# Kernel tuning notes

Hardware: AMD Instinct MI355X
Metric: run time of the kernel (lower is better)

## Reference

```python
import jax, jax.numpy as jnp
import numpy as np

N = 100000      # nodes
E = 1600000     # edges (no self loops; GATv2Conv adds them)
D_NODE = 256    # node_embedding_depth
D_MSG = 128     # message_depth
D_RBF = 32      # radial_dim
H = 8           # heads
D_HEAD = D_MSG // H


def setup_inputs() -> dict:
    key = jax.random.key(0)
    ks = jax.random.split(key, 12)
    x = jax.random.normal(ks[0], (N, D_NODE), dtype=jnp.float32)
    rbf = jax.random.uniform(ks[1], (E, D_RBF), dtype=jnp.float32)
    # edges with no self loops: src = (dst + r) % N, r in [1, N)
    dst = jax.random.randint(ks[2], (E,), 0, N)
    r = jax.random.randint(ks[3], (E,), 1, N)
    src = (dst + r) % N
    edge_index = jnp.stack([src, dst]).astype(jnp.int64)
    batch = jnp.zeros((N,), dtype=jnp.int64)
    s = 0.05
    W_n2m = jax.random.normal(ks[4], (D_MSG, D_NODE), dtype=jnp.float32) * s
    W_r2m = jax.random.normal(ks[5], (D_MSG, D_RBF), dtype=jnp.float32) * s
    Wl = jax.random.normal(ks[6], (D_MSG, D_MSG), dtype=jnp.float32) * s
    bl = jnp.zeros((D_MSG,), dtype=jnp.float32)
    Wr = jax.random.normal(ks[7], (D_MSG, D_MSG), dtype=jnp.float32) * s
    br = jnp.zeros((D_MSG,), dtype=jnp.float32)
    We = jax.random.normal(ks[8], (D_MSG, D_MSG), dtype=jnp.float32) * s
    att = jax.random.normal(ks[9], (H, D_HEAD), dtype=jnp.float32) * s
    bias = jnp.zeros((D_MSG,), dtype=jnp.float32)
    W_m2n = jax.random.normal(ks[10], (D_NODE, D_MSG), dtype=jnp.float32) * s
    return {"x": x, "rbf": rbf, "edge_index": edge_index, "batch": batch,
            "W_n2m": W_n2m, "W_r2m": W_r2m, "Wl": Wl, "bl": bl, "Wr": Wr,
            "br": br, "We": We, "att": att, "bias": bias, "W_m2n": W_m2n}


def reference(x, rbf, edge_index, batch, W_n2m, W_r2m, Wl, bl, Wr, br, We, att, bias, W_m2n):
    n = x.shape[0]
    h, d = att.shape
    # node_to_message / radial_to_message (norm=None -> identity Normalization)
    xm = x @ W_n2m.T                      # [N, D_MSG]
    ea = rbf @ W_r2m.T                    # [E, D_MSG]
    src, dst = edge_index[0], edge_index[1]
    # GATv2Conv add_self_loops with fill_value='mean': self-loop edge_attr is
    # the mean of incoming edge attrs per target node (0 if none).
    deg = jax.ops.segment_sum(jnp.ones((ea.shape[0],), ea.dtype), dst, num_segments=n)
    loop_attr = jax.ops.segment_sum(ea, dst, num_segments=n) / jnp.maximum(deg, 1.0)[:, None]
    loop_idx = jnp.arange(n, dtype=src.dtype)
    src_f = jnp.concatenate([src, loop_idx])
    dst_f = jnp.concatenate([dst, loop_idx])
    ea_f = jnp.concatenate([ea, loop_attr], axis=0)   # [E+N, D_MSG]
    # GATv2 attention
    xl = (xm @ Wl.T + bl).reshape(n, h, d)            # source transform
    xr = (xm @ Wr.T + br).reshape(n, h, d)            # target transform
    e = (ea_f @ We.T).reshape(-1, h, d)               # edge transform
    u = jax.nn.leaky_relu(xl[src_f] + xr[dst_f] + e, 0.2)  # [E+N, H, d]
    logits = jnp.einsum('ehd,hd->eh', u, att)         # [E+N, H]
    # segment softmax over incoming edges per target node (self loops guarantee non-empty)
    mx = jax.ops.segment_max(logits, dst_f, num_segments=n)
    p = jnp.exp(logits - mx[dst_f])
    denom = jax.ops.segment_sum(p, dst_f, num_segments=n)
    alpha = p / denom[dst_f]                          # [E+N, H]
    msg = xl[src_f] * alpha[:, :, None]               # [E+N, H, d]
    out = jax.ops.segment_sum(msg, dst_f, num_segments=n).reshape(n, h * d) + bias
    return out @ W_m2n.T                              # [N, D_NODE]
```

## Files before the change

### kernel.cpp

```cpp
#include <hip/hip_runtime.h>
#include <cstdint>
#include <cstddef>

#define N_NODES 100000
#define N_EDGES 1600000

#define M_PAD 100096
#define SCAN_NB 98
#define CH 16

#define OFF_XLR    ((size_t)0)
#define OFF_XB     (OFF_XLR    + (size_t)N_NODES*256)
#define OFF_ACCB   (OFF_XB     + (size_t)12812288)
#define OFF_CSRS   (OFF_ACCB   + (size_t)6406144)
#define OFF_CSRE   (OFF_CSRS   + (size_t)N_EDGES)
#define OFF_ROW    (OFF_CSRE   + (size_t)N_EDGES)
#define OFF_CNT    (OFF_ROW    + (size_t)100016)
#define OFF_DEGI   (OFF_CNT    + (size_t)N_NODES)
#define OFF_BSUMS  (OFF_DEGI   + (size_t)N_NODES)
#define OFF_BCAT   (OFF_BSUMS  + 128)
#define OFF_WCOMBB (OFF_BCAT   + 256)
#define OFF_WCATB  (OFF_WCOMBB + 2048)
#define OFF_WM2NB  (OFF_WCATB  + 32768)

typedef __attribute__((ext_vector_type(8))) short short8;
typedef __attribute__((ext_vector_type(4))) float float4v;

__device__ __forceinline__ unsigned short f2bf(float f) {
  unsigned u = __float_as_uint(f);
  unsigned r = (u + 0x7fff + ((u >> 16) & 1)) >> 16;
  return (unsigned short)r;
}

__global__ void k_zero(float* __restrict__ p, size_t n4) {
  size_t i = (size_t)blockIdx.x * blockDim.x + threadIdx.x;
  size_t stride = (size_t)gridDim.x * blockDim.x;
  float4 z = make_float4(0.f, 0.f, 0.f, 0.f);
  for (; i < n4; i += stride) ((float4*)p)[i] = z;
}

__global__ void k_convx(const float* __restrict__ x, unsigned short* __restrict__ xb, unsigned n4) {
  unsigned i = blockIdx.x * blockDim.x + threadIdx.x;
  unsigned stride = gridDim.x * blockDim.x;
  for (; i < n4; i += stride) {
    float4 v = ((const float4*)x)[i];
    ushort4 o;
    o.x = f2bf(v.x); o.y = f2bf(v.y); o.z = f2bf(v.z); o.w = f2bf(v.w);
    ((ushort4*)xb)[i] = o;
  }
}

__global__ void k_weights(const float* __restrict__ Wl, const float* __restrict__ Wr,
                          const float* __restrict__ We, const float* __restrict__ W_n2m,
                          const float* __restrict__ W_r2m, const float* __restrict__ bl,
                          const float* __restrict__ br, const float* __restrict__ W_m2n,
                          unsigned short* __restrict__ WcatB, float* __restrict__ bcat,
                          unsigned short* __restrict__ WcombB, unsigned short* __restrict__ Wm2nB) {
  int idx = blockIdx.x * blockDim.x + threadIdx.x;
  if (idx < 65536) {
    int o = idx >> 8, i = idx & 255;
    const float* wrow = (o < 128) ? (Wl + o * 128) : (Wr + (o - 128) * 128);
    float s = 0.f;
    for (int k = 0; k < 128; ++k) s += wrow[k] * W_n2m[k * 256 + i];
    WcatB[idx] = f2bf(s);
  } else if (idx < 65536 + 256) {
    int o = idx - 65536;
    bcat[o] = (o < 128) ? bl[o] : br[o - 128];
  } else if (idx < 65536 + 256 + 4096) {
    int q = idx - (65536 + 256);
    int j = q >> 7, o = q & 127;
    float s = 0.f;
    for (int k = 0; k < 128; ++k) s += We[o * 128 + k] * W_r2m[k * 32 + j];
    WcombB[o * 32 + j] = f2bf(s);
  } else if (idx < 65536 + 256 + 4096 + 32768) {
    int q = idx - (65536 + 256 + 4096);
    Wm2nB[q] = f2bf(W_m2n[q]);
  }
}

template <bool HAS_BIAS>
__global__ __launch_bounds__(256) void gemm_mfma(const unsigned short* __restrict__ A,
                                                 const unsigned short* __restrict__ B,
                                                 const float* __restrict__ bias,
                                                 float* __restrict__ C,
                                                 int M, int NC, int K) {
  __shared__ short As[128 * 32];
  __shared__ short Bs[128 * 32];
  const int tid = threadIdx.x;
  const int lane = tid & 63;
  const int wv = tid >> 6;
  const int rowBase = blockIdx.x << 7;
  const int colBase = blockIdx.y << 7;
  const int wrow = (wv & 1) << 6;
  const int wcol = (wv >> 1) << 6;

  const int srow = tid >> 2;
  const int skc = (tid & 3) << 3;

  const int n0 = lane & 15;
  const int q = lane >> 4;

  float4v acc[4][4];
#pragma unroll
  for (int i = 0; i < 4; ++i)
#pragma unroll
    for (int j = 0; j < 4; ++j) acc[i][j] = (float4v)(0.f);

  for (int k0 = 0; k0 < K; k0 += 32) {
    const unsigned aoff0 = (unsigned)(rowBase + srow) * K + k0 + skc;
    const unsigned aoff1 = (unsigned)(rowBase + 64 + srow) * K + k0 + skc;
    const unsigned boff0 = (unsigned)(colBase + srow) * K + k0 + skc;
    const unsigned boff1 = (unsigned)(colBase + 64 + srow) * K + k0 + skc;
    uint4 a0 = *(const uint4*)(A + aoff0);
    uint4 a1 = *(const uint4*)(A + aoff1);
    uint4 b0 = *(const uint4*)(B + boff0);
    uint4 b1 = *(const uint4*)(B + boff1);
    __syncthreads();
    ((uint4*)As)[tid] = a0;
    ((uint4*)As)[256 + tid] = a1;
    ((uint4*)Bs)[tid] = b0;
    ((uint4*)Bs)[256 + tid] = b1;
    __syncthreads();

    short8 af[4], bf[4];
    const short8* Ap = (const short8*)As;
    const short8* Bp = (const short8*)Bs;
#pragma unroll
    for (int i = 0; i < 4; ++i) af[i] = Ap[(wrow + i * 16 + n0) * 4 + q];
#pragma unroll
    for (int j = 0; j < 4; ++j) bf[j] = Bp[(wcol + j * 16 + n0) * 4 + q];
#pragma unroll
    for (int i = 0; i < 4; ++i)
#pragma unroll
      for (int j = 0; j < 4; ++j)
        acc[i][j] = __builtin_amdgcn_mfma_f32_16x16x32_bf16(af[i], bf[j], acc[i][j], 0, 0, 0);
  }

#pragma unroll
  for (int j = 0; j < 4; ++j) {
    const int col = colBase + wcol + j * 16 + n0;
    const float bv = HAS_BIAS ? bias[col] : 0.f;
#pragma unroll
    for (int i = 0; i < 4; ++i) {
      const int row0 = rowBase + wrow + i * 16 + (q << 2);
#pragma unroll
      for (int r = 0; r < 4; ++r) {
        const int row = row0 + r;
        if (row < M) C[(unsigned)row * NC + col] = acc[i][j][r] + bv;
      }
    }
  }
}

__global__ void k_hist(const int* __restrict__ dst, int* __restrict__ degi) {
  unsigned e = blockIdx.x * blockDim.x + threadIdx.x;
  if (e < N_EDGES) atomicAdd(&degi[dst[e]], 1);
}

__global__ __launch_bounds__(1024) void k_scan1(const int* __restrict__ degi,
                                                int* __restrict__ row,
                                                int* __restrict__ bsums) {
  __shared__ int sm[1024];
  const int tid = threadIdx.x;
  const unsigned i = blockIdx.x * 1024 + tid;
  int v = (i < N_NODES) ? degi[i] : 0;
  sm[tid] = v;
  __syncthreads();
  for (int d = 1; d < 1024; d <<= 1) {
    int t = (tid >= d) ? sm[tid - d] : 0;
    __syncthreads();
    sm[tid] += t;
    __syncthreads();
  }
  int incl = sm[tid];
  if (i < N_NODES) row[i] = incl - v;
  if (tid == 1023) bsums[blockIdx.x] = incl;
}

__global__ void k_scan2(int* __restrict__ bsums) {
  __shared__ int sm[SCAN_NB];
  const int tid = threadIdx.x;
  if (tid < SCAN_NB) sm[tid] = bsums[tid];
  __syncthreads();
  if (tid == 0) {
    int run = 0;
    for (int b = 0; b < SCAN_NB; ++b) { int t = sm[b]; sm[b] = run; run += t; }
  }
  __syncthreads();
  if (tid < SCAN_NB) bsums[tid] = sm[tid];
}

__global__ __launch_bounds__(1024) void k_scan3(int* __restrict__ row,
                                                const int* __restrict__ bsums) {
  const unsigned i = blockIdx.x * 1024 + threadIdx.x;
  if (i < N_NODES) row[i] += bsums[blockIdx.x];
  if (i == 0) row[N_NODES] = N_EDGES;
}

__global__ void k_scatter(const int* __restrict__ src, const int* __restrict__ dst,
                          const int* __restrict__ row, int* __restrict__ cnt,
                          int* __restrict__ csrs, int* __restrict__ csre) {
  unsigned e = blockIdx.x * blockDim.x + threadIdx.x;
  if (e < N_EDGES) {
    int d = dst[e];
    int pos = row[d] + atomicAdd(&cnt[d], 1);
    csrs[pos] = src[e];
    csre[pos] = (int)e;
  }
}

__global__ __launch_bounds__(128) void k_node(
    const float* __restrict__ XLR, const float* __restrict__ rbf,
    const int* __restrict__ csrs, const int* __restrict__ csre,
    const int* __restrict__ row, const unsigned short* __restrict__ WcombB,
    const float* __restrict__ att, const float* __restrict__ bias,
    unsigned short* __restrict__ accb) {
  __shared__ __align__(16) float et_s[CH][132];
  __shared__ int src_s[CH];
  __shared__ int eid_s[CH];
  const int tid = threadIdx.x;
  const int lane = tid & 63;
  const int wv = tid >> 6;
  const int n0 = lane & 15;
  const int q = lane >> 4;
  const int wcol = wv << 6;
  const unsigned n = blockIdx.x;

  const float att_r = att[tid];
  const int off = row[n], end = row[n + 1];
  const float xl_d = XLR[(n << 8) + tid];
  const float xr_d = XLR[(n << 8) + 128 + tid];

  short8 bfr[4];
#pragma unroll
  for (int j = 0; j < 4; ++j)
    bfr[j] = *(const short8*)(WcombB + (wcol + j * 16 + n0) * 32 + (q << 3));

  float S = 0.f, den = 0.f, etacc = 0.f;

  for (int c0 = off; c0 < end; c0 += CH) {
    const int cnt = min(CH, end - c0);
    __syncthreads();
    if (tid < cnt) { src_s[tid] = csrs[c0 + tid]; eid_s[tid] = csre[c0 + tid]; }
    __syncthreads();
    short8 af = (short8)0;
    if (n0 < cnt) {
      const float* rp = rbf + (size_t)(unsigned)eid_s[n0] * 32 + (q << 3);
      float4 v0 = ((const float4*)rp)[0];
      float4 v1 = ((const float4*)rp)[1];
      af[0] = (short)f2bf(v0.x); af[1] = (short)f2bf(v0.y);
      af[2] = (short)f2bf(v0.z); af[3] = (short)f2bf(v0.w);
      af[4] = (short)f2bf(v1.x); af[5] = (short)f2bf(v1.y);
      af[6] = (short)f2bf(v1.z); af[7] = (short)f2bf(v1.w);
    }
    float4v c[4];
#pragma unroll
    for (int j = 0; j < 4; ++j)
      c[j] = __builtin_amdgcn_mfma_f32_16x16x32_bf16(af, bfr[j], (float4v)(0.f), 0, 0, 0);
#pragma unroll
    for (int j = 0; j < 4; ++j)
#pragma unroll
      for (int r = 0; r < 4; ++r)
        et_s[(q << 2) + r][wcol + j * 16 + n0] = c[j][r];
    __syncthreads();
#pragma unroll 2
    for (int i = 0; i < cnt; ++i) {
      const unsigned s = (unsigned)src_s[i];
      const float et = et_s[i][tid];
      const float xls = XLR[(s << 8) + tid];
      float u = xls + xr_d + et;
      u = (u > 0.f) ? u : 0.2f * u;
      float r = u * att_r;
      r += __shfl_xor(r, 1);
      r += __shfl_xor(r, 2);
      r += __shfl_xor(r, 4);
      r += __shfl_xor(r, 8);
      const float p = __expf(r);
      den += p;
      S += p * xls;
      etacc += et;
    }
  }

  const float inv = 1.f / fmaxf((float)(end - off), 1.f);
  float u = xl_d + xr_d + etacc * inv;
  u = (u > 0.f) ? u : 0.2f * u;
  float r = u * att_r;
  r += __shfl_xor(r, 1);
  r += __shfl_xor(r, 2);
  r += __shfl_xor(r, 4);
  r += __shfl_xor(r, 8);
  const float p = __expf(r);
  den += p;
  S += p * xl_d;

  const float outv = S / den + bias[tid];
  accb[((size_t)n << 7) + tid] = f2bf(outv);
}

extern "C" void kernel_launch(void* const* d_in, const int* in_sizes, int n_in,
                              void* d_out, int out_size, void* d_ws, size_t ws_size,
                              hipStream_t stream) {
  const float* x     = (const float*)d_in[0];
  const float* rbf   = (const float*)d_in[1];
  const int*   ei    = (const int*)d_in[2];
  const float* W_n2m = (const float*)d_in[4];
  const float* W_r2m = (const float*)d_in[5];
  const float* Wl    = (const float*)d_in[6];
  const float* bl    = (const float*)d_in[7];
  const float* Wr    = (const float*)d_in[8];
  const float* br    = (const float*)d_in[9];
  const float* We    = (const float*)d_in[10];
  const float* att   = (const float*)d_in[11];
  const float* bias  = (const float*)d_in[12];
  const float* W_m2n = (const float*)d_in[13];
  float* out = (float*)d_out;
  float* ws  = (float*)d_ws;

  const int* src = ei;
  const int* dst = ei + N_EDGES;

  float* XLR    = ws + OFF_XLR;
  unsigned short* xb    = (unsigned short*)(ws + OFF_XB);
  unsigned short* accb  = (unsigned short*)(ws + OFF_ACCB);
  int* csrs   = (int*)(ws + OFF_CSRS);
  int* csre   = (int*)(ws + OFF_CSRE);
  int* rowoff = (int*)(ws + OFF_ROW);
  int* cnt    = (int*)(ws + OFF_CNT);
  int* degi   = (int*)(ws + OFF_DEGI);
  int* bsums  = (int*)(ws + OFF_BSUMS);
  float* bcat   = ws + OFF_BCAT;
  unsigned short* WcombB = (unsigned short*)(ws + OFF_WCOMBB);
  unsigned short* WcatB = (unsigned short*)(ws + OFF_WCATB);
  unsigned short* Wm2nB = (unsigned short*)(ws + OFF_WM2NB);

  k_weights<<<401, 256, 0, stream>>>(Wl, Wr, We, W_n2m, W_r2m, bl, br, W_m2n,
                                     WcatB, bcat, WcombB, Wm2nB);
  k_convx<<<2048, 256, 0, stream>>>(x, xb, (unsigned)(N_NODES * 256 / 4));
  gemm_mfma<true><<<dim3(M_PAD / 128, 2), 256, 0, stream>>>(
      xb, WcatB, bcat, XLR, N_NODES, 256, 256);
  k_zero<<<196, 256, 0, stream>>>(ws + OFF_CNT, 50000);
  k_hist<<<N_EDGES / 256, 256, 0, stream>>>(dst, degi);
  k_scan1<<<SCAN_NB, 1024, 0, stream>>>(degi, rowoff, bsums);
  k_scan2<<<1, 128, 0, stream>>>(bsums);
  k_scan3<<<SCAN_NB, 1024, 0, stream>>>(rowoff, bsums);
  k_scatter<<<N_EDGES / 256, 256, 0, stream>>>(src, dst, rowoff, cnt, csrs, csre);
  k_node<<<N_NODES, 128, 0, stream>>>(XLR, rbf, csrs, csre, rowoff, WcombB,
                                      att, bias, accb);
  gemm_mfma<false><<<dim3(M_PAD / 128, 2), 256, 0, stream>>>(
      accb, Wm2nB, nullptr, out, N_NODES, 256, 128);
}
```

Baseline: 965.3 us.

## Fuse preprocessing kernels, decoupled-lookback scan, packed CSR, prefetch source rows

Several changes at once. Weight prep and counter zeroing merge into one kernel. The x-to-bf16 conversion moves into the first GEMM's A load. The three-kernel scan becomes one ticket-ordered chained scan with acquire/release flags. CSR src and edge id are packed into one int2 array. In k_node, edge indices are broadcast by shuffle instead of through shared memory, and all 16 source rows of a chunk are prefetched into registers before use. Together these cut launches, extra passes over memory and barriers, at the cost of spin-waiting in the scan and more register pressure in k_node.

```diff
diff --git a/kernel.cpp b/kernel.cpp
--- a/kernel.cpp
+++ b/kernel.cpp
@@ -10,15 +10,13 @@
 #define CH 16
 
 #define OFF_XLR    ((size_t)0)
-#define OFF_XB     (OFF_XLR    + (size_t)N_NODES*256)
-#define OFF_ACCB   (OFF_XB     + (size_t)12812288)
-#define OFF_CSRS   (OFF_ACCB   + (size_t)6406144)
-#define OFF_CSRE   (OFF_CSRS   + (size_t)N_EDGES)
-#define OFF_ROW    (OFF_CSRE   + (size_t)N_EDGES)
+#define OFF_ACCB   (OFF_XLR    + (size_t)N_NODES*256)
+#define OFF_CSRSE  (OFF_ACCB   + (size_t)6406144)
+#define OFF_ROW    (OFF_CSRSE  + (size_t)3200000)
 #define OFF_CNT    (OFF_ROW    + (size_t)100016)
 #define OFF_DEGI   (OFF_CNT    + (size_t)N_NODES)
-#define OFF_BSUMS  (OFF_DEGI   + (size_t)N_NODES)
-#define OFF_BCAT   (OFF_BSUMS  + 128)
+#define OFF_FLAGS  (OFF_DEGI   + (size_t)N_NODES)
+#define OFF_BCAT   (OFF_FLAGS  + 128)
 #define OFF_WCOMBB (OFF_BCAT   + 256)
 #define OFF_WCATB  (OFF_WCOMBB + 2048)
 #define OFF_WM2NB  (OFF_WCATB  + 32768)
@@ -32,31 +30,31 @@
   return (unsigned short)r;
 }
 
-__global__ void k_zero(float* __restrict__ p, size_t n4) {
-  size_t i = (size_t)blockIdx.x * blockDim.x + threadIdx.x;
-  size_t stride = (size_t)gridDim.x * blockDim.x;
-  float4 z = make_float4(0.f, 0.f, 0.f, 0.f);
-  for (; i < n4; i += stride) ((float4*)p)[i] = z;
-}
-
-__global__ void k_convx(const float* __restrict__ x, unsigned short* __restrict__ xb, unsigned n4) {
-  unsigned i = blockIdx.x * blockDim.x + threadIdx.x;
-  unsigned stride = gridDim.x * blockDim.x;
-  for (; i < n4; i += stride) {
-    float4 v = ((const float4*)x)[i];
-    ushort4 o;
-    o.x = f2bf(v.x); o.y = f2bf(v.y); o.z = f2bf(v.z); o.w = f2bf(v.w);
-    ((ushort4*)xb)[i] = o;
-  }
-}
-
-__global__ void k_weights(const float* __restrict__ Wl, const float* __restrict__ Wr,
-                          const float* __restrict__ We, const float* __restrict__ W_n2m,
-                          const float* __restrict__ W_r2m, const float* __restrict__ bl,
-                          const float* __restrict__ br, const float* __restrict__ W_m2n,
-                          unsigned short* __restrict__ WcatB, float* __restrict__ bcat,
-                          unsigned short* __restrict__ WcombB, unsigned short* __restrict__ Wm2nB) {
-  int idx = blockIdx.x * blockDim.x + threadIdx.x;
+__device__ __forceinline__ uint4 pack8(float4 a, float4 b) {
+  uint4 r;
+  r.x = (unsigned)f2bf(a.x) | ((unsigned)f2bf(a.y) << 16);
+  r.y = (unsigned)f2bf(a.z) | ((unsigned)f2bf(a.w) << 16);
+  r.z = (unsigned)f2bf(b.x) | ((unsigned)f2bf(b.y) << 16);
+  r.w = (unsigned)f2bf(b.z) | ((unsigned)f2bf(b.w) << 16);
+  return r;
+}
+
+__global__ __launch_bounds__(256) void k_pre(
+    const float* __restrict__ Wl, const float* __restrict__ Wr,
+    const float* __restrict__ We, const float* __restrict__ W_n2m,
+    const float* __restrict__ W_r2m, const float* __restrict__ bl,
+    const float* __restrict__ br, const float* __restrict__ W_m2n,
+    unsigned short* __restrict__ WcatB, float* __restrict__ bcat,
+    unsigned short* __restrict__ WcombB, unsigned short* __restrict__ Wm2nB,
+    float* __restrict__ zbase) {
+  const int b = blockIdx.x;
+  const int tid = threadIdx.x;
+  if (b >= 401) {
+    unsigned i = (unsigned)(b - 401) * 256u + tid;
+    if (i < 50032u) ((float4*)zbase)[i] = make_float4(0.f, 0.f, 0.f, 0.f);
+    return;
+  }
+  int idx = b * 256 + tid;
   if (idx < 65536) {
     int o = idx >> 8, i = idx & 255;
     const float* wrow = (o < 128) ? (Wl + o * 128) : (Wr + (o - 128) * 128);
@@ -78,8 +76,8 @@
   }
 }
 
-template <bool HAS_BIAS>
-__global__ __launch_bounds__(256) void gemm_mfma(const unsigned short* __restrict__ A,
+template <bool HAS_BIAS, bool A_F32>
+__global__ __launch_bounds__(256) void gemm_mfma(const void* __restrict__ Av,
                                                  const unsigned short* __restrict__ B,
                                                  const float* __restrict__ bias,
                                                  float* __restrict__ C,
@@ -107,14 +105,24 @@
     for (int j = 0; j < 4; ++j) acc[i][j] = (float4v)(0.f);
 
   for (int k0 = 0; k0 < K; k0 += 32) {
-    const unsigned aoff0 = (unsigned)(rowBase + srow) * K + k0 + skc;
-    const unsigned aoff1 = (unsigned)(rowBase + 64 + srow) * K + k0 + skc;
-    const unsigned boff0 = (unsigned)(colBase + srow) * K + k0 + skc;
-    const unsigned boff1 = (unsigned)(colBase + 64 + srow) * K + k0 + skc;
-    uint4 a0 = *(const uint4*)(A + aoff0);
-    uint4 a1 = *(const uint4*)(A + aoff1);
-    uint4 b0 = *(const uint4*)(B + boff0);
-    uint4 b1 = *(const uint4*)(B + boff1);
+    uint4 a0, a1;
+    if (A_F32) {
+      const float* Af = (const float*)Av;
+      const int r0 = min(rowBase + srow, M - 1);
+      const int r1 = min(rowBase + 64 + srow, M - 1);
+      const float* p0 = Af + (size_t)r0 * K + k0 + skc;
+      const float* p1 = Af + (size_t)r1 * K + k0 + skc;
+      float4 x0 = ((const float4*)p0)[0], x1 = ((const float4*)p0)[1];
+      float4 y0 = ((const float4*)p1)[0], y1 = ((const float4*)p1)[1];
+      a0 = pack8(x0, x1);
+      a1 = pack8(y0, y1);
+    } else {
+      const unsigned short* Ab = (const unsigned short*)Av;
+      a0 = *(const uint4*)(Ab + (size_t)(unsigned)(rowBase + srow) * K + k0 + skc);
+      a1 = *(const uint4*)(Ab + (size_t)(unsigned)(rowBase + 64 + srow) * K + k0 + skc);
+    }
+    uint4 b0 = *(const uint4*)(B + (size_t)(unsigned)(colBase + srow) * K + k0 + skc);
+    uint4 b1 = *(const uint4*)(B + (size_t)(unsigned)(colBase + 64 + srow) * K + k0 + skc);
     __syncthreads();
     ((uint4*)As)[tid] = a0;
     ((uint4*)As)[256 + tid] = a1;
@@ -157,12 +165,17 @@
   if (e < N_EDGES) atomicAdd(&degi[dst[e]], 1);
 }
 
-__global__ __launch_bounds__(1024) void k_scan1(const int* __restrict__ degi,
-                                                int* __restrict__ row,
-                                                int* __restrict__ bsums) {
+__global__ __launch_bounds__(1024) void k_scan(const int* __restrict__ degi,
+                                               int* __restrict__ row,
+                                               int* __restrict__ flags,
+                                               int* __restrict__ ticket) {
   __shared__ int sm[1024];
+  __shared__ int sh_b, sh_prev;
   const int tid = threadIdx.x;
-  const unsigned i = blockIdx.x * 1024 + tid;
+  if (tid == 0) sh_b = atomicAdd(ticket, 1);
+  __syncthreads();
+  const int b = sh_b;
+  const unsigned i = (unsigned)b * 1024u + tid;
   int v = (i < N_NODES) ? degi[i] : 0;
   sm[tid] = v;
   __syncthreads();
@@ -172,52 +185,46 @@
     sm[tid] += t;
     __syncthreads();
   }
-  int incl = sm[tid];
-  if (i < N_NODES) row[i] = incl - v;
-  if (tid == 1023) bsums[blockIdx.x] = incl;
-}
-
-__global__ void k_scan2(int* __restrict__ bsums) {
-  __shared__ int sm[SCAN_NB];
-  const int tid = threadIdx.x;
-  if (tid < SCAN_NB) sm[tid] = bsums[tid];
+  const int incl = sm[tid];
+  const int total = sm[1023];
+  if (tid == 0) {
+    int prev = 0;
+    if (b > 0) {
+      int f;
+      while ((f = __hip_atomic_load(&flags[b - 1], __ATOMIC_ACQUIRE,
+                                    __HIP_MEMORY_SCOPE_AGENT)) == 0) {
+        __builtin_amdgcn_s_sleep(1);
+      }
+      prev = f - 1;
+    }
+    __hip_atomic_store(&flags[b], prev + total + 1, __ATOMIC_RELEASE,
+                       __HIP_MEMORY_SCOPE_AGENT);
+    sh_prev = prev;
+  }
   __syncthreads();
-  if (tid == 0) {
-    int run = 0;
-    for (int b = 0; b < SCAN_NB; ++b) { int t = sm[b]; sm[b] = run; run += t; }
-  }
-  __syncthreads();
-  if (tid < SCAN_NB) bsums[tid] = sm[tid];
-}
-
-__global__ __launch_bounds__(1024) void k_scan3(int* __restrict__ row,
-                                                const int* __restrict__ bsums) {
-  const unsigned i = blockIdx.x * 1024 + threadIdx.x;
-  if (i < N_NODES) row[i] += bsums[blockIdx.x];
-  if (i == 0) row[N_NODES] = N_EDGES;
+  const int base = sh_prev;
+  if (i < N_NODES) row[i] = base + incl - v;
+  if (b == 0 && tid == 0) row[N_NODES] = N_EDGES;
 }
 
 __global__ void k_scatter(const int* __restrict__ src, const int* __restrict__ dst,
                           const int* __restrict__ row, int* __restrict__ cnt,
-                          int* __restrict__ csrs, int* __restrict__ csre) {
+                          int2* __restrict__ csrse) {
   unsigned e = blockIdx.x * blockDim.x + threadIdx.x;
   if (e < N_EDGES) {
     int d = dst[e];
     int pos = row[d] + atomicAdd(&cnt[d], 1);
-    csrs[pos] = src[e];
-    csre[pos] = (int)e;
+    csrse[pos] = make_int2(src[e], (int)e);
   }
 }
 
 __global__ __launch_bounds__(128) void k_node(
     const float* __restrict__ XLR, const float* __restrict__ rbf,
-    const int* __restrict__ csrs, const int* __restrict__ csre,
-    const int* __restrict__ row, const unsigned short* __restrict__ WcombB,
+    const int2* __restrict__ csrse, const int* __restrict__ row,
+    const unsigned short* __restrict__ WcombB,
     const float* __restrict__ att, const float* __restrict__ bias,
     unsigned short* __restrict__ accb) {
   __shared__ __align__(16) float et_s[CH][132];
-  __shared__ int src_s[CH];
-  __shared__ int eid_s[CH];
   const int tid = threadIdx.x;
   const int lane = tid & 63;
   const int wv = tid >> 6;
@@ -240,12 +247,15 @@
 
   for (int c0 = off; c0 < end; c0 += CH) {
     const int cnt = min(CH, end - c0);
-    __syncthreads();
-    if (tid < cnt) { src_s[tid] = csrs[c0 + tid]; eid_s[tid] = csre[c0 + tid]; }
-    __syncthreads();
+    int sreg = 0, ereg = 0;
+    if (lane < cnt) {
+      int2 se = csrse[c0 + lane];
+      sreg = se.x; ereg = se.y;
+    }
+    const int e_n0 = __shfl(ereg, n0);
     short8 af = (short8)0;
     if (n0 < cnt) {
-      const float* rp = rbf + (size_t)(unsigned)eid_s[n0] * 32 + (q << 3);
+      const float* rp = rbf + (size_t)(unsigned)e_n0 * 32 + (q << 3);
       float4 v0 = ((const float4*)rp)[0];
       float4 v1 = ((const float4*)rp)[1];
       af[0] = (short)f2bf(v0.x); af[1] = (short)f2bf(v0.y);
@@ -257,28 +267,36 @@
 #pragma unroll
     for (int j = 0; j < 4; ++j)
       c[j] = __builtin_amdgcn_mfma_f32_16x16x32_bf16(af, bfr[j], (float4v)(0.f), 0, 0, 0);
+    __syncthreads();
 #pragma unroll
     for (int j = 0; j < 4; ++j)
 #pragma unroll
       for (int r = 0; r < 4; ++r)
         et_s[(q << 2) + r][wcol + j * 16 + n0] = c[j][r];
-    __syncthreads();
-#pragma unroll 2
-    for (int i = 0; i < cnt; ++i) {
-      const unsigned s = (unsigned)src_s[i];
-      const float et = et_s[i][tid];
-      const float xls = XLR[(s << 8) + tid];
-      float u = xls + xr_d + et;
-      u = (u > 0.f) ? u : 0.2f * u;
-      float r = u * att_r;
-      r += __shfl_xor(r, 1);
-      r += __shfl_xor(r, 2);
-      r += __shfl_xor(r, 4);
-      r += __shfl_xor(r, 8);
-      const float p = __expf(r);
-      den += p;
-      S += p * xls;
-      etacc += et;
+    float xlr[CH];
+#pragma unroll
+    for (int i = 0; i < CH; ++i) {
+      const unsigned s = (unsigned)__shfl(sreg, i);
+      xlr[i] = XLR[(s << 8) + tid];
+    }
+    __syncthreads();
+#pragma unroll
+    for (int i = 0; i < CH; ++i) {
+      if (i < cnt) {
+        const float et = et_s[i][tid];
+        const float xls = xlr[i];
+        float u = xls + xr_d + et;
+        u = (u > 0.f) ? u : 0.2f * u;
+        float r = u * att_r;
+        r += __shfl_xor(r, 1);
+        r += __shfl_xor(r, 2);
+        r += __shfl_xor(r, 4);
+        r += __shfl_xor(r, 8);
+        const float p = __expf(r);
+        den += p;
+        S += p * xls;
+        etacc += et;
+      }
     }
   }
 
@@ -321,32 +339,27 @@
   const int* dst = ei + N_EDGES;
 
   float* XLR    = ws + OFF_XLR;
-  unsigned short* xb    = (unsigned short*)(ws + OFF_XB);
-  unsigned short* accb  = (unsigned short*)(ws + OFF_ACCB);
-  int* csrs   = (int*)(ws + OFF_CSRS);
-  int* csre   = (int*)(ws + OFF_CSRE);
-  int* rowoff = (int*)(ws + OFF_ROW);
-  int* cnt    = (int*)(ws + OFF_CNT);
-  int* degi   = (int*)(ws + OFF_DEGI);
-  int* bsums  = (int*)(ws + OFF_BSUMS);
-  float* bcat   = ws + OFF_BCAT;
+  unsigned short* accb = (unsigned short*)(ws + OFF_ACCB);
+  int2* csrse  = (int2*)(ws + OFF_CSRSE);
+  int* rowoff  = (int*)(ws + OFF_ROW);
+  int* cnt     = (int*)(ws + OFF_CNT);
+  int* degi    = (int*)(ws + OFF_DEGI);
+  int* flags   = (int*)(ws + OFF_FLAGS);
+  int* ticket  = flags + 100;
+  float* bcat  = ws + OFF_BCAT;
   unsigned short* WcombB = (unsigned short*)(ws + OFF_WCOMBB);
-  unsigned short* WcatB = (unsigned short*)(ws + OFF_WCATB);
-  unsigned short* Wm2nB = (unsigned short*)(ws + OFF_WM2NB);
-
-  k_weights<<<401, 256, 0, stream>>>(Wl, Wr, We, W_n2m, W_r2m, bl, br, W_m2n,
-                                     WcatB, bcat, WcombB, Wm2nB);
-  k_convx<<<2048, 256, 0, stream>>>(x, xb, (unsigned)(N_NODES * 256 / 4));
-  gemm_mfma<true><<<dim3(M_PAD / 128, 2), 256, 0, stream>>>(
-      xb, WcatB, bcat, XLR, N_NODES, 256, 256);
-  k_zero<<<196, 256, 0, stream>>>(ws + OFF_CNT, 50000);
+  unsigned short* WcatB  = (unsigned short*)(ws + OFF_WCATB);
+  unsigned short* Wm2nB  = (unsigned short*)(ws + OFF_WM2NB);
+
+  k_pre<<<597, 256, 0, stream>>>(Wl, Wr, We, W_n2m, W_r2m, bl, br, W_m2n,
+                                 WcatB, bcat, WcombB, Wm2nB, ws + OFF_CNT);
   k_hist<<<N_EDGES / 256, 256, 0, stream>>>(dst, degi);
-  k_scan1<<<SCAN_NB, 1024, 0, stream>>>(degi, rowoff, bsums);
-  k_scan2<<<1, 128, 0, stream>>>(bsums);
-  k_scan3<<<SCAN_NB, 1024, 0, stream>>>(rowoff, bsums);
-  k_scatter<<<N_EDGES / 256, 256, 0, stream>>>(src, dst, rowoff, cnt, csrs, csre);
-  k_node<<<N_NODES, 128, 0, stream>>>(XLR, rbf, csrs, csre, rowoff, WcombB,
+  k_scan<<<SCAN_NB, 1024, 0, stream>>>(degi, rowoff, flags, ticket);
+  k_scatter<<<N_EDGES / 256, 256, 0, stream>>>(src, dst, rowoff, cnt, csrse);
+  gemm_mfma<true, true><<<dim3(M_PAD / 128, 2), 256, 0, stream>>>(
+      x, WcatB, bcat, XLR, N_NODES, 256, 256);
+  k_node<<<N_NODES, 128, 0, stream>>>(XLR, rbf, csrse, rowoff, WcombB,
                                       att, bias, accb);
-  gemm_mfma<false><<<dim3(M_PAD / 128, 2), 256, 0, stream>>>(
+  gemm_mfma<false, false><<<dim3(M_PAD / 128, 2), 256, 0, stream>>>(
       accb, Wm2nB, nullptr, out, N_NODES, 256, 128);
 }
```

Result: slower. 1.057 ms (+9.5%).
